# Kernel optimization log

Hardware: AMD Instinct MI355X
Metric: run time of the kernel (lower is better)

## Reference

```python
import jax, jax.numpy as jnp
import numpy as np

DIM = 512
NSLOTS = 8
ITERS = 3
EPS = 1e-8
LN_EPS = 1e-5
SCALE = DIM ** -0.5


def _ln(x, g, b):
    m = jnp.mean(x, axis=-1, keepdims=True)
    v = jnp.mean((x - m) ** 2, axis=-1, keepdims=True)
    return (x - m) / jnp.sqrt(v + LN_EPS) * g + b


def _gru(x, h, W_ih, W_hh, b_ih, b_hh):
    # PyTorch GRUCell, gate order r,z,n
    gi = x @ W_ih.T + b_ih
    gh = h @ W_hh.T + b_hh
    ir, iz, inn = jnp.split(gi, 3, axis=-1)
    hr, hz, hn = jnp.split(gh, 3, axis=-1)
    r = jax.nn.sigmoid(ir + hr)
    z = jax.nn.sigmoid(iz + hz)
    n = jnp.tanh(inn + r * hn)
    return (1.0 - z) * n + z * h


def _norm_attn(dots):
    # softmax over slot axis, then renormalize over token axis
    a = jax.nn.softmax(dots, axis=1)
    return a / (jnp.sum(a, axis=-1, keepdims=True) + EPS)


def setup_inputs() -> dict:
    key = jax.random.key(0)
    ks = jax.random.split(key, 16)
    b, na, ni = 32, 1024, 3136
    d, hd = DIM, DIM  # hidden_dim = max(dim, 128) = 512
    s = 0.02
    inp = {
        'inputs_audio': jax.random.normal(ks[0], (b, na, d), jnp.float32),
        'inputs_image': jax.random.normal(ks[1], (b, ni, d), jnp.float32),
        'slots_noise': jax.random.normal(ks[2], (b, NSLOTS, d), jnp.float32),
        'slots_mu': jax.random.normal(ks[3], (1, 1, d), jnp.float32),
        'slots_logsigma': jnp.zeros((1, 1, d), jnp.float32),
        'ln_in_g': jnp.ones((d,), jnp.float32), 'ln_in_b': jnp.zeros((d,), jnp.float32),
        'ln_slots_g': jnp.ones((d,), jnp.float32), 'ln_slots_b': jnp.zeros((d,), jnp.float32),
        'ln_ff_g': jnp.ones((d,), jnp.float32), 'ln_ff_b': jnp.zeros((d,), jnp.float32),
        'Wq': jax.random.normal(ks[4], (d, d), jnp.float32) * s, 'bq': jnp.zeros((d,), jnp.float32),
        'Wk': jax.random.normal(ks[5], (d, d), jnp.float32) * s, 'bk': jnp.zeros((d,), jnp.float32),
        'Wv': jax.random.normal(ks[6], (d, d), jnp.float32) * s, 'bv': jnp.zeros((d,), jnp.float32),
        'W_ih': jax.random.normal(ks[7], (3 * d, d), jnp.float32) * s,
        'W_hh': jax.random.normal(ks[8], (3 * d, d), jnp.float32) * s,
        'b_ih': jnp.zeros((3 * d,), jnp.float32), 'b_hh': jnp.zeros((3 * d,), jnp.float32),
        'W1': jax.random.normal(ks[9], (hd, d), jnp.float32) * s, 'b1': jnp.zeros((hd,), jnp.float32),
        'W2': jax.random.normal(ks[10], (d, hd), jnp.float32) * s, 'b2': jnp.zeros((d,), jnp.float32),
    }
    return inp


def reference(inputs_audio, inputs_image, slots_noise, slots_mu, slots_logsigma,
              ln_in_g, ln_in_b, ln_slots_g, ln_slots_b, ln_ff_g, ln_ff_b,
              Wq, bq, Wk, bk, Wv, bv, W_ih, W_hh, b_ih, b_hh, W1, b1, W2, b2):
    b, na, d = inputs_audio.shape
    slots0 = slots_mu + jnp.exp(slots_logsigma) * slots_noise  # [b, S, d]

    ia = _ln(inputs_audio, ln_in_g, ln_in_b)
    ii = _ln(inputs_image, ln_in_g, ln_in_b)
    k_a = ia @ Wk.T + bk
    v_a = ia @ Wv.T + bv
    k_i = ii @ Wk.T + bk
    v_i = ii @ Wv.T + bv

    def mlp(x):
        return jax.nn.relu(x @ W1.T + b1) @ W2.T + b2

    def step(slots, k, v):
        prev = slots
        sn = _ln(slots, ln_slots_g, ln_slots_b)
        q = sn @ Wq.T + bq
        dots = jnp.einsum('bid,bjd->bij', q, k) * SCALE
        attn = _norm_attn(dots)
        upd = jnp.einsum('bjd,bij->bid', v, attn)
        h = _gru(upd.reshape(-1, d), prev.reshape(-1, d), W_ih, W_hh, b_ih, b_hh)
        slots = h.reshape(b, -1, d)
        slots = slots + mlp(_ln(slots, ln_ff_g, ln_ff_b))
        return slots, q, attn

    slots_a, slots_i = slots0, slots0
    for _ in range(ITERS):
        slots_a, q_a, attn_a = step(slots_a, k_a, v_a)
        slots_i, q_i, attn_i = step(slots_i, k_i, v_i)

    cross_ai = _norm_attn(jnp.einsum('bid,bjd->bij', q_a, k_i) * SCALE)  # audio->image
    cross_ia = _norm_attn(jnp.einsum('bid,bjd->bij', q_i, k_a) * SCALE)  # image->audio

    return (slots_a, q_a, k_a, attn_a, cross_ia,
            slots_i, q_i, k_i, attn_i, cross_ai)
```

## Files before the change

kernel.cpp:

```cpp
#include <hip/hip_runtime.h>
#include <hip/hip_bf16.h>

#define DIM 512
#define EPS 1e-8f
#define LN_EPS 1e-5f
#define SCALE 0.04419417382415922f

typedef float f32x4 __attribute__((ext_vector_type(4)));
typedef __bf16 bf16;
typedef __bf16 bf16x8 __attribute__((ext_vector_type(8)));

typedef const __attribute__((address_space(1))) void gvoid;
typedef __attribute__((address_space(3))) void lvoid;

__device__ inline float bf2f_lo(unsigned u) { union { unsigned x; float f; } c; c.x = u << 16; return c.f; }
__device__ inline float bf2f_hi(unsigned u) { union { unsigned x; float f; } c; c.x = u & 0xffff0000u; return c.f; }

__global__ __launch_bounds__(256) void k_stats_convert(
    const float* __restrict__ x, bf16* __restrict__ xbf,
    float* __restrict__ stats, int M)
{
  int row = blockIdx.x * 4 + (threadIdx.x >> 6);
  int lane = threadIdx.x & 63;
  if (row >= M) return;
  const float* xr = x + (size_t)row * DIM;
  float4 a = *(const float4*)(xr + lane * 8);
  float4 b = *(const float4*)(xr + lane * 8 + 4);
  float s  = a.x + a.y + a.z + a.w + b.x + b.y + b.z + b.w;
  float ss = a.x*a.x + a.y*a.y + a.z*a.z + a.w*a.w
           + b.x*b.x + b.y*b.y + b.z*b.z + b.w*b.w;
  for (int off = 32; off; off >>= 1) { s += __shfl_xor(s, off); ss += __shfl_xor(ss, off); }
  float mean = s * (1.0f / DIM);
  float var  = ss * (1.0f / DIM) - mean * mean;
  float rs   = rsqrtf(var + LN_EPS);
  if (lane == 0) { stats[row * 2] = mean; stats[row * 2 + 1] = rs; }
  union { bf16 h[8]; uint4 u; } cv;
  cv.h[0] = (bf16)a.x; cv.h[1] = (bf16)a.y; cv.h[2] = (bf16)a.z; cv.h[3] = (bf16)a.w;
  cv.h[4] = (bf16)b.x; cv.h[5] = (bf16)b.y; cv.h[6] = (bf16)b.z; cv.h[7] = (bf16)b.w;
  *(uint4*)(xbf + (size_t)row * DIM + lane * 8) = cv.u;
}

__global__ __launch_bounds__(256) void k_stats512(
    const float* __restrict__ x, float* __restrict__ stats)
{
  int row = blockIdx.x * 4 + (threadIdx.x >> 6);
  int lane = threadIdx.x & 63;
  const float* xr = x + (size_t)row * DIM;
  float4 a = *(const float4*)(xr + lane * 8);
  float4 b = *(const float4*)(xr + lane * 8 + 4);
  float s  = a.x + a.y + a.z + a.w + b.x + b.y + b.z + b.w;
  float ss = a.x*a.x + a.y*a.y + a.z*a.z + a.w*a.w
           + b.x*b.x + b.y*b.y + b.z*b.z + b.w*b.w;
  for (int off = 32; off; off >>= 1) { s += __shfl_xor(s, off); ss += __shfl_xor(ss, off); }
  float mean = s * (1.0f / DIM);
  float rs   = rsqrtf(ss * (1.0f / DIM) - mean * mean + LN_EPS);
  if (lane == 0) { stats[row * 2] = mean; stats[row * 2 + 1] = rs; }
}

__global__ __launch_bounds__(64) void k_prep(
    const float* __restrict__ Wk, const float* __restrict__ bk,
    const float* __restrict__ Wv, const float* __restrict__ bv,
    const float* __restrict__ g_in, const float* __restrict__ b_in,
    const float* __restrict__ Wq, const float* __restrict__ bq,
    const float* __restrict__ g_s, const float* __restrict__ b_s,
    const float* __restrict__ W1, const float* __restrict__ b1,
    const float* __restrict__ g_f, const float* __restrict__ b_f,
    bf16* __restrict__ wbf, float* __restrict__ c1kv, float* __restrict__ c2kv,
    float* __restrict__ Wqp, float* __restrict__ cq1, float* __restrict__ cq2,
    float* __restrict__ W1p, float* __restrict__ cf1, float* __restrict__ cf2)
{
  int n = blockIdx.x; int lane = threadIdx.x;
  if (n < 1024) {
    const float* W = (n < DIM) ? (Wk + (size_t)n * DIM) : (Wv + (size_t)(n - DIM) * DIM);
    float bias = (n < DIM) ? bk[n] : bv[n - DIM];
    float s1 = 0.f, s2 = 0.f;
    union { bf16 h[8]; uint4 u; } cv;
#pragma unroll
    for (int j = 0; j < 8; ++j) {
      int d = lane * 8 + j;
      float w = W[d];
      float gw = g_in[d] * w;
      s1 += gw; s2 += b_in[d] * w;
      cv.h[j] = (bf16)gw;
    }
    *(uint4*)(wbf + (size_t)n * DIM + lane * 8) = cv.u;
    for (int off = 32; off; off >>= 1) { s1 += __shfl_xor(s1, off); s2 += __shfl_xor(s2, off); }
    if (lane == 0) { c1kv[n] = s1; c2kv[n] = s2 + bias; }
  } else {
    int m; const float* W; float bias; const float* g; const float* b;
    float* Wp; float* cc1; float* cc2;
    if (n < 1536) { m = n - 1024; W = Wq + (size_t)m * DIM; bias = bq[m]; g = g_s; b = b_s; Wp = Wqp; cc1 = cq1; cc2 = cq2; }
    else          { m = n - 1536; W = W1 + (size_t)m * DIM; bias = b1[m]; g = g_f; b = b_f; Wp = W1p; cc1 = cf1; cc2 = cf2; }
    float s1 = 0.f, s2 = 0.f;
    float arr[8];
#pragma unroll
    for (int j = 0; j < 8; ++j) {
      int d = lane * 8 + j;
      float w = W[d];
      float gw = g[d] * w;
      s1 += gw; s2 += b[d] * w;
      arr[j] = gw;
    }
    *(float4*)(Wp + (size_t)m * DIM + lane * 8)     = make_float4(arr[0], arr[1], arr[2], arr[3]);
    *(float4*)(Wp + (size_t)m * DIM + lane * 8 + 4) = make_float4(arr[4], arr[5], arr[6], arr[7]);
    for (int off = 32; off; off >>= 1) { s1 += __shfl_xor(s1, off); s2 += __shfl_xor(s2, off); }
    if (lane == 0) { cc1[m] = s1; cc2[m] = s2 + bias; }
  }
}

__global__ __launch_bounds__(256, 4) void k_kv_gemm(
    const bf16* __restrict__ xa, const bf16* __restrict__ xi,
    const bf16* __restrict__ wbf,
    const float* __restrict__ sa, const float* __restrict__ si,
    const float* __restrict__ c1, const float* __restrict__ c2,
    float* __restrict__ ka, float* __restrict__ ki,
    bf16* __restrict__ kba, bf16* __restrict__ kbi,
    bf16* __restrict__ va, bf16* __restrict__ vi,
    int nblkA, int nblkTot)
{
  __shared__ bf16 As[2][128 * 32];
  __shared__ bf16 Bs[2][128 * 32];
  const int t = threadIdx.x, wave = t >> 6, lane = t & 63;
  int bid = blockIdx.x;
  int rid = (bid & 7) * (nblkTot >> 3) + (bid >> 3);
  bool isA = rid < nblkA;
  int lrid = isA ? rid : rid - nblkA;
  const bf16* x = isA ? xa : xi;
  const float* stats = isA ? sa : si;
  float* kout = isA ? ka : ki;
  bf16* kbf = isA ? kba : kbi;
  bf16* vbf = isA ? va : vi;
  const int row0 = (lrid >> 3) * 128, col0 = (lrid & 7) * 128;
  f32x4 acc[4][4] = {};

  const int sr  = wave * 16 + (lane >> 2);
  const int sgl = ((lane & 3) ^ ((lane >> 3) & 3)) * 8;
  const bf16* asrc = x   + (size_t)(row0 + sr) * DIM + sgl;
  const bf16* bsrc = wbf + (size_t)(col0 + sr) * DIM + sgl;

  auto stage = [&](int buf, int k0) {
#pragma unroll
    for (int p = 0; p < 2; ++p) {
      __builtin_amdgcn_global_load_lds(
          (gvoid*)(asrc + (size_t)(p * 64) * DIM + k0),
          (lvoid*)((char*)&As[buf][0] + (p * 256 + wave * 64) * 16), 16, 0, 0);
      __builtin_amdgcn_global_load_lds(
          (gvoid*)(bsrc + (size_t)(p * 64) * DIM + k0),
          (lvoid*)((char*)&Bs[buf][0] + (p * 256 + wave * 64) * 16), 16, 0, 0);
    }
  };

  const int l15 = lane & 15, q16 = lane >> 4;
  const int wm = wave >> 1, wn = wave & 1;
  const int gpx = (q16 ^ ((l15 >> 1) & 3)) * 8;

  stage(0, 0);
  int cur = 0;
  for (int ks = 0; ks < 16; ++ks) {
    __syncthreads();
    if (ks < 15) stage(cur ^ 1, (ks + 1) * 32);
    const bf16* Ab = &As[cur][0];
    const bf16* Bb = &Bs[cur][0];
    bf16x8 ax[4], bw[4];
#pragma unroll
    for (int mi = 0; mi < 4; ++mi)
      ax[mi] = *(const bf16x8*)(Ab + (wm * 64 + mi * 16 + l15) * 32 + gpx);
#pragma unroll
    for (int ni = 0; ni < 4; ++ni)
      bw[ni] = *(const bf16x8*)(Bb + (wn * 64 + ni * 16 + l15) * 32 + gpx);
#pragma unroll
    for (int ni = 0; ni < 4; ++ni)
#pragma unroll
      for (int mi = 0; mi < 4; ++mi)
        acc[ni][mi] = __builtin_amdgcn_mfma_f32_16x16x32_bf16(bw[ni], ax[mi], acc[ni][mi], 0, 0, 0);
    cur ^= 1;
  }

#pragma unroll
  for (int mi = 0; mi < 4; ++mi) {
    int row = row0 + wm * 64 + mi * 16 + l15;
    float2 st = *(const float2*)&stats[row * 2];
    float rs = st.y, rm = st.y * st.x;
#pragma unroll
    for (int ni = 0; ni < 4; ++ni) {
      int col = col0 + wn * 64 + ni * 16 + q16 * 4;
      float4 c1v = *(const float4*)&c1[col];
      float4 c2v = *(const float4*)&c2[col];
      f32x4 a = acc[ni][mi];
      float4 o;
      o.x = rs * a[0] - rm * c1v.x + c2v.x;
      o.y = rs * a[1] - rm * c1v.y + c2v.y;
      o.z = rs * a[2] - rm * c1v.z + c2v.z;
      o.w = rs * a[3] - rm * c1v.w + c2v.w;
      union { bf16 h[4]; uint2 u; } pk;
      pk.h[0] = (bf16)o.x; pk.h[1] = (bf16)o.y; pk.h[2] = (bf16)o.z; pk.h[3] = (bf16)o.w;
      if (col0 < DIM) {
        *(float4*)&kout[(size_t)row * DIM + col] = o;
        if (kbf) *(uint2*)&kbf[(size_t)row * DIM + col] = pk.u;
      } else {
        *(uint2*)&vbf[(size_t)row * DIM + (col - DIM)] = pk.u;
      }
    }
  }
}

__global__ __launch_bounds__(256) void k_f2bf(
    const float* __restrict__ in, bf16* __restrict__ out)
{
  size_t i = ((size_t)blockIdx.x * 256 + threadIdx.x) * 8;
  float4 a = *(const float4*)(in + i);
  float4 b = *(const float4*)(in + i + 4);
  union { bf16 h[8]; uint4 u; } cv;
  cv.h[0] = (bf16)a.x; cv.h[1] = (bf16)a.y; cv.h[2] = (bf16)a.z; cv.h[3] = (bf16)a.w;
  cv.h[4] = (bf16)b.x; cv.h[5] = (bf16)b.y; cv.h[6] = (bf16)b.z; cv.h[7] = (bf16)b.w;
  *(uint4*)(out + i) = cv.u;
}

__global__ __launch_bounds__(256) void k_init_slots(
    const float* __restrict__ noise, const float* __restrict__ mu,
    const float* __restrict__ lsig, float* __restrict__ slots)
{
  int idx = blockIdx.x * 256 + threadIdx.x;
  int d = idx & (DIM - 1);
  float v = mu[d] + expf(lsig[d]) * noise[idx];
  slots[idx] = v;
  slots[131072 + idx] = v;
}

template <int MODE>
__global__ __launch_bounds__(128) void k_sgemm(
    const float* __restrict__ A, const float* __restrict__ B, int N,
    float* __restrict__ C,
    const float* __restrict__ c1a, const float* __restrict__ c2a,
    const float* __restrict__ stats,
    const float* __restrict__ bias, const float* __restrict__ invden,
    const float* __restrict__ R,
    float* __restrict__ outA, float* __restrict__ outI,
    bf16* __restrict__ qbf)
{
  __shared__ float As[32][33];
  __shared__ float Bs[64][33];
  int t = threadIdx.x;
  int m0 = blockIdx.y * 32, n0 = blockIdx.x * 64;
  float acc[4][4] = {};
  for (int k0 = 0; k0 < DIM; k0 += 32) {
    __syncthreads();
#pragma unroll
    for (int p = 0; p < 2; ++p) {
      int idx = p * 128 + t, r = idx >> 3, c4 = (idx & 7) * 4;
      float4 v = *(const float4*)(A + (size_t)(m0 + r) * DIM + k0 + c4);
      As[r][c4] = v.x; As[r][c4 + 1] = v.y; As[r][c4 + 2] = v.z; As[r][c4 + 3] = v.w;
    }
#pragma unroll
    for (int p = 0; p < 4; ++p) {
      int idx = p * 128 + t, r = idx >> 3, c4 = (idx & 7) * 4;
      float4 v = *(const float4*)(B + (size_t)(n0 + r) * DIM + k0 + c4);
      Bs[r][c4] = v.x; Bs[r][c4 + 1] = v.y; Bs[r][c4 + 2] = v.z; Bs[r][c4 + 3] = v.w;
    }
    __syncthreads();
    int tr = t >> 4, tc = t & 15;
#pragma unroll
    for (int k = 0; k < 32; ++k) {
      float a0 = As[tr * 4][k], a1 = As[tr * 4 + 1][k], a2 = As[tr * 4 + 2][k], a3 = As[tr * 4 + 3][k];
      float b0 = Bs[tc * 4][k], b1 = Bs[tc * 4 + 1][k], b2 = Bs[tc * 4 + 2][k], b3 = Bs[tc * 4 + 3][k];
      acc[0][0] += a0 * b0; acc[0][1] += a0 * b1; acc[0][2] += a0 * b2; acc[0][3] += a0 * b3;
      acc[1][0] += a1 * b0; acc[1][1] += a1 * b1; acc[1][2] += a1 * b2; acc[1][3] += a1 * b3;
      acc[2][0] += a2 * b0; acc[2][1] += a2 * b1; acc[2][2] += a2 * b2; acc[2][3] += a2 * b3;
      acc[3][0] += a3 * b0; acc[3][1] += a3 * b1; acc[3][2] += a3 * b2; acc[3][3] += a3 * b3;
    }
  }
  int tr = t >> 4, tc = t & 15;
#pragma unroll
  for (int mi = 0; mi < 4; ++mi) {
    int row = m0 + tr * 4 + mi;
#pragma unroll
    for (int ni = 0; ni < 4; ++ni) {
      int col = n0 + tc * 4 + ni;
      float v = acc[mi][ni];
      if (MODE == 0 || MODE == 3) {
        float mean = stats[row * 2], rs = stats[row * 2 + 1];
        v = rs * v - rs * mean * c1a[col] + c2a[col];
      }
      if (MODE == 1) v = v * invden[row] + bias[col];
      if (MODE == 2 || MODE == 4) v += bias[col];
      if (MODE == 3) v = fmaxf(v, 0.0f);
      if (MODE == 4) v += R[(size_t)row * N + col];
      if (MODE == 0) {
        if (row < 256) outA[(size_t)row * DIM + col] = v;
        else           outI[(size_t)(row - 256) * DIM + col] = v;
        qbf[(size_t)row * DIM + col] = (bf16)(v * SCALE);
      } else {
        C[(size_t)row * N + col] = v;
        if (MODE == 4 && outA) {
          if (row < 256) outA[(size_t)row * DIM + col] = v;
          else           outI[(size_t)(row - 256) * DIM + col] = v;
        }
      }
    }
  }
}

__global__ __launch_bounds__(256) void k_dots(
    const bf16* __restrict__ qA, const bf16* __restrict__ qI,
    const bf16* __restrict__ kA, const bf16* __restrict__ kI,
    float* __restrict__ aoutA, float* __restrict__ aoutI,
    float* __restrict__ denp, int NA_, int NI_)
{
  __shared__ bf16 ks[128 * 64];
  __shared__ float dsh[32];
  int t = threadIdx.x, wave = t >> 6, lane = t & 63;
  int b = blockIdx.y, tile = blockIdx.x;
  bool isA = tile < 8;
  int til = isA ? tile : tile - 8;
  int N = isA ? NA_ : NI_;
  int j0 = til * 128;
  const bf16* q = (isA ? qA : qI) + (size_t)b * 8 * DIM;
  const bf16* k = (isA ? kA : kI) + (size_t)b * N * DIM;
  float* aout = (isA ? aoutA : aoutI) + (size_t)b * 8 * N;
  int drow = (isA ? 0 : 256) + b * 8;

  const int l15 = lane & 15, q16 = lane >> 4;
  bf16x8 afq[16];
  {
    const bf16* qr = q + (size_t)(l15 & 7) * DIM + q16 * 8;
#pragma unroll
    for (int f = 0; f < 16; ++f)
      afq[f] = *(const bf16x8*)(qr + f * 32);
  }

  const int sr  = wave * 8 + (lane >> 3);
  const int sgl = ((lane & 7) ^ (lane >> 3)) * 8;
  f32x4 acc[2] = {};
  for (int c = 0; c < 8; ++c) {
    __syncthreads();
#pragma unroll
    for (int p = 0; p < 4; ++p) {
      int jr = j0 + p * 32 + sr;
      if (jr > N - 1) jr = N - 1;
      __builtin_amdgcn_global_load_lds(
          (gvoid*)(k + (size_t)jr * DIM + c * 64 + sgl),
          (lvoid*)((char*)ks + (p * 256 + wave * 64) * 16), 16, 0, 0);
    }
    __syncthreads();
#pragma unroll
    for (int kk = 0; kk < 2; ++kk) {
#pragma unroll
      for (int n = 0; n < 2; ++n) {
        int R = wave * 32 + n * 16 + l15;
        int gp = (kk * 4 + q16) ^ (R & 7);
        bf16x8 bfr = *(const bf16x8*)(ks + R * 64 + gp * 8);
        acc[n] = __builtin_amdgcn_mfma_f32_16x16x32_bf16(afq[c * 2 + kk], bfr, acc[n], 0, 0, 0);
      }
    }
  }

  float dsum[8];
#pragma unroll
  for (int i = 0; i < 8; ++i) dsum[i] = 0.f;
#pragma unroll
  for (int n = 0; n < 2; ++n) {
    int j = j0 + wave * 32 + n * 16 + l15;
    float dv[8];
#pragma unroll
    for (int r = 0; r < 4; ++r) {
      float own = acc[n][r];
      float oth = __shfl_xor(own, 16);
      if (q16 == 0) { dv[r] = own; dv[4 + r] = oth; }
      else          { dv[r] = oth; dv[4 + r] = own; }
    }
    float mx = dv[0];
#pragma unroll
    for (int i = 1; i < 8; ++i) mx = fmaxf(mx, dv[i]);
    float sum = 0.f;
#pragma unroll
    for (int i = 0; i < 8; ++i) { dv[i] = __expf(dv[i] - mx); sum += dv[i]; }
    float inv = 1.0f / sum;
    bool valid = (j < N);
#pragma unroll
    for (int i = 0; i < 8; ++i) {
      float av = valid ? dv[i] * inv : 0.0f;
      dsum[i] += av;
      if (valid && q16 == 0) aout[(size_t)i * N + j] = av;
    }
  }
#pragma unroll
  for (int i = 0; i < 8; ++i) {
    float v = dsum[i];
    v += __shfl_xor(v, 1); v += __shfl_xor(v, 2);
    v += __shfl_xor(v, 4); v += __shfl_xor(v, 8);
    dsum[i] = v;
  }
  if (lane == 0) {
#pragma unroll
    for (int i = 0; i < 8; ++i) dsh[wave * 8 + i] = dsum[i];
  }
  __syncthreads();
  if (t < 8) {
    float den = dsh[t] + dsh[8 + t] + dsh[16 + t] + dsh[24 + t];
    denp[((size_t)drow + t) * 32 + til] = den;
  }
}

__global__ __launch_bounds__(256) void k_upd(
    const bf16* __restrict__ vA, const bf16* __restrict__ vI,
    const float* __restrict__ aA, const float* __restrict__ aI,
    float* __restrict__ numpA, float* __restrict__ numpI, int NA_, int NI_)
{
  __shared__ float ash[128 * 12];
  int t = threadIdx.x, b = blockIdx.y, x = blockIdx.x;
  bool isA = x < 4;
  int c = isA ? x : x - 4;
  int N = isA ? NA_ : NI_;
  int nc = isA ? 4 : 13;
  int jstart = c * 256;
  int jend = jstart + 256; if (jend > N) jend = N;
  const bf16* v = (isA ? vA : vI) + (size_t)b * N * DIM;
  const float* a = (isA ? aA : aI) + (size_t)b * 8 * N;
  float acc[16] = {};
  int d0 = t * 2;
  for (int jt = jstart; jt < jend; jt += 128) {
    int jmax = jend - jt; if (jmax > 128) jmax = 128;
    __syncthreads();
    {
      int i = t >> 5, jq = (t & 31) * 4;
      float4 av = make_float4(0.f, 0.f, 0.f, 0.f);
      if (jt + jq < N) av = *(const float4*)&a[(size_t)i * N + jt + jq];
      ash[(jq + 0) * 12 + i] = av.x;
      ash[(jq + 1) * 12 + i] = av.y;
      ash[(jq + 2) * 12 + i] = av.z;
      ash[(jq + 3) * 12 + i] = av.w;
    }
    __syncthreads();
    for (int jj = 0; jj < jmax; ++jj) {
      unsigned vv = *(const unsigned*)(v + (size_t)(jt + jj) * DIM + d0);
      float v0 = bf2f_lo(vv), v1 = bf2f_hi(vv);
      float4 a0 = *(const float4*)&ash[jj * 12];
      float4 a1 = *(const float4*)&ash[jj * 12 + 4];
      acc[0]  += a0.x * v0; acc[1]  += a0.x * v1;
      acc[2]  += a0.y * v0; acc[3]  += a0.y * v1;
      acc[4]  += a0.z * v0; acc[5]  += a0.z * v1;
      acc[6]  += a0.w * v0; acc[7]  += a0.w * v1;
      acc[8]  += a1.x * v0; acc[9]  += a1.x * v1;
      acc[10] += a1.y * v0; acc[11] += a1.y * v1;
      acc[12] += a1.z * v0; acc[13] += a1.z * v1;
      acc[14] += a1.w * v0; acc[15] += a1.w * v1;
    }
  }
  float* np = (isA ? numpA : numpI) + (((size_t)b * nc + c) * 8) * DIM;
#pragma unroll
  for (int i = 0; i < 8; ++i)
    *(float2*)&np[(size_t)i * DIM + d0] = make_float2(acc[i * 2], acc[i * 2 + 1]);
}

__global__ __launch_bounds__(256) void k_numred(
    const float* __restrict__ numpA, const float* __restrict__ numpI,
    const float* __restrict__ denp,
    float* __restrict__ num, float* __restrict__ invden)
{
  int m = blockIdx.x, t = threadIdx.x;
  bool isA = m < 256;
  int mm = isA ? m : m - 256;
  int bb = mm >> 3, i = mm & 7;
  int nc = isA ? 4 : 13;
  const float* np = (isA ? numpA : numpI) + (((size_t)bb * nc) * 8 + i) * DIM;
  int d0 = t * 2;
  float s0 = 0.f, s1 = 0.f;
  for (int c = 0; c < nc; ++c) {
    float2 vv = *(const float2*)&np[(size_t)c * 8 * DIM + d0];
    s0 += vv.x; s1 += vv.y;
  }
  *(float2*)&num[(size_t)m * DIM + d0] = make_float2(s0, s1);
  if (t == 0) {
    int nch = isA ? 8 : 25;
    float den = EPS;
    for (int c2 = 0; c2 < nch; ++c2) den += denp[(size_t)m * 32 + c2];
    invden[m] = 1.0f / den;
  }
}

__global__ __launch_bounds__(256) void k_gru(
    const float* __restrict__ gi, const float* __restrict__ gh,
    const float* __restrict__ prev,
    float* __restrict__ hout, float* __restrict__ stats_h)
{
  int m = blockIdx.x; int t = threadIdx.x;
  size_t b3 = (size_t)m * 1536, b1 = (size_t)m * DIM;
  float h[2]; float s = 0.f, ss = 0.f;
#pragma unroll
  for (int p = 0; p < 2; ++p) {
    int d = t + p * 256;
    float ir = gi[b3 + d], iz = gi[b3 + 512 + d], in_ = gi[b3 + 1024 + d];
    float hr = gh[b3 + d], hz = gh[b3 + 512 + d], hn = gh[b3 + 1024 + d];
    float r = 1.f / (1.f + __expf(-(ir + hr)));
    float z = 1.f / (1.f + __expf(-(iz + hz)));
    float n = tanhf(in_ + r * hn);
    float hv = (1.f - z) * n + z * prev[b1 + d];
    hout[b1 + d] = hv;
    h[p] = hv; s += hv; ss += hv * hv;
  }
  for (int off = 32; off; off >>= 1) { s += __shfl_xor(s, off); ss += __shfl_xor(ss, off); }
  __shared__ float red[8];
  int wv = t >> 6, ln = t & 63;
  if (ln == 0) { red[wv] = s; red[4 + wv] = ss; }
  __syncthreads();
  s = red[0] + red[1] + red[2] + red[3];
  ss = red[4] + red[5] + red[6] + red[7];
  float mean = s * (1.0f / DIM);
  float rs = rsqrtf(ss * (1.0f / DIM) - mean * mean + LN_EPS);
  if (t == 0) { stats_h[m * 2] = mean; stats_h[m * 2 + 1] = rs; }
}

__global__ __launch_bounds__(256) void k_renorm2(
    const float* __restrict__ aA, const float* __restrict__ aI,
    const float* __restrict__ denp,
    float* __restrict__ outA, float* __restrict__ outI, int NA_, int NI_)
{
  int m = blockIdx.x; int t = threadIdx.x;
  bool isA = m < 256;
  int mm = isA ? m : m - 256;
  int N = isA ? NA_ : NI_;
  int nch = isA ? 8 : 25;
  const float* in = (isA ? aA : aI) + (size_t)mm * N;
  float* out = (isA ? outA : outI) + (size_t)mm * N;
  float den = EPS;
  for (int c = 0; c < nch; ++c) den += denp[(size_t)m * 32 + c];
  float inv = 1.0f / den;
  for (int idx = t; idx * 4 < N; idx += 256) {
    float4 v = *(const float4*)&in[idx * 4];
    v.x *= inv; v.y *= inv; v.z *= inv; v.w *= inv;
    *(float4*)&out[idx * 4] = v;
  }
}

extern "C" void kernel_launch(void* const* d_in, const int* in_sizes, int n_in,
                              void* d_out, int out_size, void* d_ws, size_t ws_size,
                              hipStream_t stream)
{
  (void)in_sizes; (void)n_in; (void)out_size;
  const float* x_a   = (const float*)d_in[0];
  const float* x_i   = (const float*)d_in[1];
  const float* noise = (const float*)d_in[2];
  const float* mu    = (const float*)d_in[3];
  const float* lsig  = (const float*)d_in[4];
  const float* ln_in_g = (const float*)d_in[5];
  const float* ln_in_b = (const float*)d_in[6];
  const float* ln_s_g  = (const float*)d_in[7];
  const float* ln_s_b  = (const float*)d_in[8];
  const float* ln_f_g  = (const float*)d_in[9];
  const float* ln_f_b  = (const float*)d_in[10];
  const float* Wq = (const float*)d_in[11]; const float* bq = (const float*)d_in[12];
  const float* Wk = (const float*)d_in[13]; const float* bk = (const float*)d_in[14];
  const float* Wv = (const float*)d_in[15]; const float* bv = (const float*)d_in[16];
  const float* W_ih = (const float*)d_in[17]; const float* W_hh = (const float*)d_in[18];
  const float* b_ih = (const float*)d_in[19]; const float* b_hh = (const float*)d_in[20];
  const float* W1 = (const float*)d_in[21]; const float* b1 = (const float*)d_in[22];
  const float* W2 = (const float*)d_in[23]; const float* b2 = (const float*)d_in[24];

  const int NA = 1024, NI = 3136;
  const int MA = 32 * NA, MI = 32 * NI;

  float* out = (float*)d_out;
  float* o_slots_a  = out;
  float* o_q_a      = out + 131072;
  float* o_k_a      = out + 262144;
  float* o_attn_a   = out + 17039360;
  float* o_cross_ia = out + 17301504;
  float* o_slots_i  = out + 17563648;
  float* o_q_i      = out + 17694720;
  float* o_k_i      = out + 17825792;
  float* o_attn_i   = out + 69206016;
  float* o_cross_ai = out + 70008832;

  char* w = (char*)d_ws;
  size_t used = 0;
  auto alloc = [&](size_t bytes) {
    char* p = w + used;
    used += (bytes + 255) & ~(size_t)255;
    return p;
  };
  bf16* xbf_a = (bf16*)alloc((size_t)MA * DIM * 2);
  bf16* xbf_i = (bf16*)alloc((size_t)MI * DIM * 2);
  bf16* vbf_a = (bf16*)alloc((size_t)MA * DIM * 2);
  bf16* vbf_i = (bf16*)alloc((size_t)MI * DIM * 2);
  float* stats_a = (float*)alloc((size_t)MA * 2 * 4);
  float* stats_i = (float*)alloc((size_t)MI * 2 * 4);
  bf16* wbf  = (bf16*)alloc(1024 * 512 * 2);
  float* c1kv = (float*)alloc(1024 * 4);
  float* c2kv = (float*)alloc(1024 * 4);
  float* Wqp = (float*)alloc(512 * 512 * 4);
  float* cq1 = (float*)alloc(512 * 4);
  float* cq2 = (float*)alloc(512 * 4);
  float* W1p = (float*)alloc(512 * 512 * 4);
  float* cf1 = (float*)alloc(512 * 4);
  float* cf2 = (float*)alloc(512 * 4);
  float* slots = (float*)alloc(512 * 512 * 4);
  bf16*  qbf   = (bf16*)alloc(512 * 512 * 2);
  float* mid   = (float*)alloc(512 * 512 * 4);
  float* hid   = (float*)alloc(512 * 512 * 4);
  float* num   = (float*)alloc(512 * 512 * 4);
  float* gib   = (float*)alloc(512 * 1536 * 4);
  float* ghb   = (float*)alloc(512 * 1536 * 4);
  float* stats_s = (float*)alloc(512 * 2 * 4);
  float* stats_h = (float*)alloc(512 * 2 * 4);
  float* invden  = (float*)alloc(512 * 4);
  float* denp    = (float*)alloc(512 * 32 * 4);
  float* abuf_a  = (float*)alloc((size_t)256 * NA * 4);
  float* abuf_i  = (float*)alloc((size_t)256 * NI * 4);
  float* numpA   = (float*)alloc((size_t)32 * 4 * 8 * DIM * 4);
  float* numpI   = (float*)alloc((size_t)32 * 13 * 8 * DIM * 4);
  if (used > ws_size) return;

  size_t kbf_bytes = (((size_t)MA * DIM * 2 + 255) & ~(size_t)255)
                   + (((size_t)MI * DIM * 2 + 255) & ~(size_t)255);
  bf16* kbf_a; bf16* kbf_i; bool kbf_fused;
  if (used + kbf_bytes <= ws_size) {
    kbf_a = (bf16*)alloc((size_t)MA * DIM * 2);
    kbf_i = (bf16*)alloc((size_t)MI * DIM * 2);
    kbf_fused = true;
  } else {
    kbf_a = xbf_a; kbf_i = xbf_i;
    kbf_fused = false;
  }

  k_stats_convert<<<MA / 4, 256, 0, stream>>>(x_a, xbf_a, stats_a, MA);
  k_stats_convert<<<MI / 4, 256, 0, stream>>>(x_i, xbf_i, stats_i, MI);
  k_prep<<<2048, 64, 0, stream>>>(Wk, bk, Wv, bv, ln_in_g, ln_in_b,
                                  Wq, bq, ln_s_g, ln_s_b, W1, b1, ln_f_g, ln_f_b,
                                  wbf, c1kv, c2kv, Wqp, cq1, cq2, W1p, cf1, cf2);
  {
    int nblkA = (MA / 128) * 8;
    int nblkTot = nblkA + (MI / 128) * 8;
    k_kv_gemm<<<nblkTot, 256, 0, stream>>>(xbf_a, xbf_i, wbf, stats_a, stats_i,
        c1kv, c2kv, o_k_a, o_k_i,
        kbf_fused ? kbf_a : nullptr, kbf_fused ? kbf_i : nullptr,
        vbf_a, vbf_i, nblkA, nblkTot);
  }
  if (!kbf_fused) {
    k_f2bf<<<MA * DIM / 2048, 256, 0, stream>>>(o_k_a, kbf_a);
    k_f2bf<<<MI * DIM / 2048, 256, 0, stream>>>(o_k_i, kbf_i);
  }
  k_init_slots<<<512, 256, 0, stream>>>(noise, mu, lsig, slots);
  k_stats512<<<128, 256, 0, stream>>>(slots, stats_s);

  for (int it = 0; it < 3; ++it) {
    bool last = (it == 2);
    k_sgemm<0><<<dim3(8, 16), 128, 0, stream>>>(slots, Wqp, DIM, nullptr,
        cq1, cq2, stats_s, nullptr, nullptr, nullptr, o_q_a, o_q_i, qbf);
    k_dots<<<dim3(33, 32), 256, 0, stream>>>(qbf, qbf + 256 * DIM,
        kbf_a, kbf_i, abuf_a, abuf_i, denp, NA, NI);
    k_upd<<<dim3(17, 32), 256, 0, stream>>>(vbf_a, vbf_i, abuf_a, abuf_i, numpA, numpI, NA, NI);
    k_numred<<<512, 256, 0, stream>>>(numpA, numpI, denp, num, invden);
    k_sgemm<1><<<dim3(24, 16), 128, 0, stream>>>(num, W_ih, 1536, gib,
        nullptr, nullptr, nullptr, b_ih, invden, nullptr, nullptr, nullptr, nullptr);
    k_sgemm<2><<<dim3(24, 16), 128, 0, stream>>>(slots, W_hh, 1536, ghb,
        nullptr, nullptr, nullptr, b_hh, nullptr, nullptr, nullptr, nullptr, nullptr);
    k_gru<<<512, 256, 0, stream>>>(gib, ghb, slots, mid, stats_h);
    k_sgemm<3><<<dim3(8, 16), 128, 0, stream>>>(mid, W1p, DIM, hid,
        cf1, cf2, stats_h, nullptr, nullptr, nullptr, nullptr, nullptr, nullptr);
    k_sgemm<4><<<dim3(8, 16), 128, 0, stream>>>(hid, W2, DIM, slots,
        nullptr, nullptr, nullptr, b2, nullptr, mid,
        last ? o_slots_a : nullptr, last ? o_slots_i : nullptr, nullptr);
    if (!last) k_stats512<<<128, 256, 0, stream>>>(slots, stats_s);
  }

  k_renorm2<<<512, 256, 0, stream>>>(abuf_a, abuf_i, denp, o_attn_a, o_attn_i, NA, NI);

  k_dots<<<dim3(33, 32), 256, 0, stream>>>(qbf + 256 * DIM, qbf,
      kbf_a, kbf_i, abuf_a, abuf_i, denp, NA, NI);
  k_renorm2<<<512, 256, 0, stream>>>(abuf_a, abuf_i, denp, o_cross_ia, o_cross_ai, NA, NI);
}
```

Before: 1.217 ms.

## Deepen prefetch in projection GEMM and dots, merge GRU gate GEMMs into one launch

The bf16 MFMA projection GEMM and the k_dots kernel now prefetch two stages ahead. Each waits with explicit vmcnt waits and scheduling barriers instead of a sync-load-sync loop, so global-to-LDS loads overlap MFMA work. k_dots gets a double-buffered LDS tile and precomputes its clamped source pointers. The two GRU gate SGEMMs (input and hidden) are merged into one k_gates launch with twice the blocks, which removes a launch and fills more CUs. The cost is extra LDS use and fragile hand-written waitcnt logic.

```diff
diff --git a/kernel.cpp b/kernel.cpp
--- a/kernel.cpp
+++ b/kernel.cpp
@@ -15,6 +15,10 @@
 
 __device__ inline float bf2f_lo(unsigned u) { union { unsigned x; float f; } c; c.x = u << 16; return c.f; }
 __device__ inline float bf2f_hi(unsigned u) { union { unsigned x; float f; } c; c.x = u & 0xffff0000u; return c.f; }
+
+#define SBAR() do { __builtin_amdgcn_sched_barrier(0); \
+                    __builtin_amdgcn_s_barrier(); \
+                    __builtin_amdgcn_sched_barrier(0); } while (0)
 
 __global__ __launch_bounds__(256) void k_stats_convert(
     const float* __restrict__ x, bf16* __restrict__ xbf,
@@ -155,10 +159,11 @@
   const int gpx = (q16 ^ ((l15 >> 1) & 3)) * 8;
 
   stage(0, 0);
+  stage(1, 32);
+  asm volatile("s_waitcnt vmcnt(4)" ::: "memory");
+  SBAR();
   int cur = 0;
   for (int ks = 0; ks < 16; ++ks) {
-    __syncthreads();
-    if (ks < 15) stage(cur ^ 1, (ks + 1) * 32);
     const bf16* Ab = &As[cur][0];
     const bf16* Bb = &Bs[cur][0];
     bf16x8 ax[4], bw[4];
@@ -173,6 +178,15 @@
 #pragma unroll
       for (int mi = 0; mi < 4; ++mi)
         acc[ni][mi] = __builtin_amdgcn_mfma_f32_16x16x32_bf16(bw[ni], ax[mi], acc[ni][mi], 0, 0, 0);
+    SBAR();
+    if (ks < 14) {
+      stage(cur, (ks + 2) * 32);
+      asm volatile("s_waitcnt vmcnt(4)" ::: "memory");
+      SBAR();
+    } else if (ks == 14) {
+      asm volatile("s_waitcnt vmcnt(0)" ::: "memory");
+      SBAR();
+    }
     cur ^= 1;
   }
 
@@ -281,8 +295,7 @@
         float mean = stats[row * 2], rs = stats[row * 2 + 1];
         v = rs * v - rs * mean * c1a[col] + c2a[col];
       }
-      if (MODE == 1) v = v * invden[row] + bias[col];
-      if (MODE == 2 || MODE == 4) v += bias[col];
+      if (MODE == 4) v += bias[col];
       if (MODE == 3) v = fmaxf(v, 0.0f);
       if (MODE == 4) v += R[(size_t)row * N + col];
       if (MODE == 0) {
@@ -300,13 +313,70 @@
   }
 }
 
+__global__ __launch_bounds__(128) void k_gates(
+    const float* __restrict__ num, const float* __restrict__ slots,
+    const float* __restrict__ Wih, const float* __restrict__ Whh,
+    const float* __restrict__ bih, const float* __restrict__ bhh,
+    const float* __restrict__ invden,
+    float* __restrict__ gib, float* __restrict__ ghb)
+{
+  bool first = blockIdx.x < 24;
+  const float* A = first ? num : slots;
+  const float* B = first ? Wih : Whh;
+  const float* bias = first ? bih : bhh;
+  float* C = first ? gib : ghb;
+  int n0 = (first ? blockIdx.x : blockIdx.x - 24) * 64;
+  int m0 = blockIdx.y * 32;
+  __shared__ float As[32][33];
+  __shared__ float Bs[64][33];
+  int t = threadIdx.x;
+  float acc[4][4] = {};
+  for (int k0 = 0; k0 < DIM; k0 += 32) {
+    __syncthreads();
+#pragma unroll
+    for (int p = 0; p < 2; ++p) {
+      int idx = p * 128 + t, r = idx >> 3, c4 = (idx & 7) * 4;
+      float4 v = *(const float4*)(A + (size_t)(m0 + r) * DIM + k0 + c4);
+      As[r][c4] = v.x; As[r][c4 + 1] = v.y; As[r][c4 + 2] = v.z; As[r][c4 + 3] = v.w;
+    }
+#pragma unroll
+    for (int p = 0; p < 4; ++p) {
+      int idx = p * 128 + t, r = idx >> 3, c4 = (idx & 7) * 4;
+      float4 v = *(const float4*)(B + (size_t)(n0 + r) * DIM + k0 + c4);
+      Bs[r][c4] = v.x; Bs[r][c4 + 1] = v.y; Bs[r][c4 + 2] = v.z; Bs[r][c4 + 3] = v.w;
+    }
+    __syncthreads();
+    int tr = t >> 4, tc = t & 15;
+#pragma unroll
+    for (int k = 0; k < 32; ++k) {
+      float a0 = As[tr * 4][k], a1 = As[tr * 4 + 1][k], a2 = As[tr * 4 + 2][k], a3 = As[tr * 4 + 3][k];
+      float b0 = Bs[tc * 4][k], b1 = Bs[tc * 4 + 1][k], b2 = Bs[tc * 4 + 2][k], b3 = Bs[tc * 4 + 3][k];
+      acc[0][0] += a0 * b0; acc[0][1] += a0 * b1; acc[0][2] += a0 * b2; acc[0][3] += a0 * b3;
+      acc[1][0] += a1 * b0; acc[1][1] += a1 * b1; acc[1][2] += a1 * b2; acc[1][3] += a1 * b3;
+      acc[2][0] += a2 * b0; acc[2][1] += a2 * b1; acc[2][2] += a2 * b2; acc[2][3] += a2 * b3;
+      acc[3][0] += a3 * b0; acc[3][1] += a3 * b1; acc[3][2] += a3 * b2; acc[3][3] += a3 * b3;
+    }
+  }
+  int tr = t >> 4, tc = t & 15;
+#pragma unroll
+  for (int mi = 0; mi < 4; ++mi) {
+    int row = m0 + tr * 4 + mi;
+    float sc = first ? invden[row] : 1.0f;
+#pragma unroll
+    for (int ni = 0; ni < 4; ++ni) {
+      int col = n0 + tc * 4 + ni;
+      C[(size_t)row * 1536 + col] = acc[mi][ni] * sc + bias[col];
+    }
+  }
+}
+
 __global__ __launch_bounds__(256) void k_dots(
     const bf16* __restrict__ qA, const bf16* __restrict__ qI,
     const bf16* __restrict__ kA, const bf16* __restrict__ kI,
     float* __restrict__ aoutA, float* __restrict__ aoutI,
     float* __restrict__ denp, int NA_, int NI_)
 {
-  __shared__ bf16 ks[128 * 64];
+  __shared__ bf16 ks[2][128 * 64];
   __shared__ float dsh[32];
   int t = threadIdx.x, wave = t >> 6, lane = t & 63;
   int b = blockIdx.y, tile = blockIdx.x;
@@ -330,28 +400,53 @@
 
   const int sr  = wave * 8 + (lane >> 3);
   const int sgl = ((lane & 7) ^ (lane >> 3)) * 8;
+  int jr = j0 + sr; if (jr > N - 1) jr = N - 1;
+  const bf16* ksrc = k + (size_t)jr * DIM + sgl;
+  int jr2 = j0 + 32 + sr; if (jr2 > N - 1) jr2 = N - 1;
+  const bf16* ksrc2 = k + (size_t)jr2 * DIM + sgl;
+  int jr3 = j0 + 64 + sr; if (jr3 > N - 1) jr3 = N - 1;
+  const bf16* ksrc3 = k + (size_t)jr3 * DIM + sgl;
+  int jr4 = j0 + 96 + sr; if (jr4 > N - 1) jr4 = N - 1;
+  const bf16* ksrc4 = k + (size_t)jr4 * DIM + sgl;
+
+  auto stage = [&](int buf, int c) {
+    __builtin_amdgcn_global_load_lds((gvoid*)(ksrc  + c * 64),
+        (lvoid*)((char*)&ks[buf][0] + (0 * 256 + wave * 64) * 16), 16, 0, 0);
+    __builtin_amdgcn_global_load_lds((gvoid*)(ksrc2 + c * 64),
+        (lvoid*)((char*)&ks[buf][0] + (1 * 256 + wave * 64) * 16), 16, 0, 0);
+    __builtin_amdgcn_global_load_lds((gvoid*)(ksrc3 + c * 64),
+        (lvoid*)((char*)&ks[buf][0] + (2 * 256 + wave * 64) * 16), 16, 0, 0);
+    __builtin_amdgcn_global_load_lds((gvoid*)(ksrc4 + c * 64),
+        (lvoid*)((char*)&ks[buf][0] + (3 * 256 + wave * 64) * 16), 16, 0, 0);
+  };
+
+  stage(0, 0);
+  stage(1, 1);
+  asm volatile("s_waitcnt vmcnt(4)" ::: "memory");
+  SBAR();
   f32x4 acc[2] = {};
+  int cur = 0;
   for (int c = 0; c < 8; ++c) {
-    __syncthreads();
-#pragma unroll
-    for (int p = 0; p < 4; ++p) {
-      int jr = j0 + p * 32 + sr;
-      if (jr > N - 1) jr = N - 1;
-      __builtin_amdgcn_global_load_lds(
-          (gvoid*)(k + (size_t)jr * DIM + c * 64 + sgl),
-          (lvoid*)((char*)ks + (p * 256 + wave * 64) * 16), 16, 0, 0);
-    }
-    __syncthreads();
 #pragma unroll
     for (int kk = 0; kk < 2; ++kk) {
 #pragma unroll
       for (int n = 0; n < 2; ++n) {
         int R = wave * 32 + n * 16 + l15;
         int gp = (kk * 4 + q16) ^ (R & 7);
-        bf16x8 bfr = *(const bf16x8*)(ks + R * 64 + gp * 8);
+        bf16x8 bfr = *(const bf16x8*)(&ks[cur][0] + R * 64 + gp * 8);
         acc[n] = __builtin_amdgcn_mfma_f32_16x16x32_bf16(afq[c * 2 + kk], bfr, acc[n], 0, 0, 0);
       }
     }
+    SBAR();
+    if (c < 6) {
+      stage(cur, c + 2);
+      asm volatile("s_waitcnt vmcnt(4)" ::: "memory");
+      SBAR();
+    } else if (c == 6) {
+      asm volatile("s_waitcnt vmcnt(0)" ::: "memory");
+      SBAR();
+    }
+    cur ^= 1;
   }
 
   float dsum[8];
@@ -650,10 +745,8 @@
         kbf_a, kbf_i, abuf_a, abuf_i, denp, NA, NI);
     k_upd<<<dim3(17, 32), 256, 0, stream>>>(vbf_a, vbf_i, abuf_a, abuf_i, numpA, numpI, NA, NI);
     k_numred<<<512, 256, 0, stream>>>(numpA, numpI, denp, num, invden);
-    k_sgemm<1><<<dim3(24, 16), 128, 0, stream>>>(num, W_ih, 1536, gib,
-        nullptr, nullptr, nullptr, b_ih, invden, nullptr, nullptr, nullptr, nullptr);
-    k_sgemm<2><<<dim3(24, 16), 128, 0, stream>>>(slots, W_hh, 1536, ghb,
-        nullptr, nullptr, nullptr, b_hh, nullptr, nullptr, nullptr, nullptr, nullptr);
+    k_gates<<<dim3(48, 16), 128, 0, stream>>>(num, slots, W_ih, W_hh,
+        b_ih, b_hh, invden, gib, ghb);
     k_gru<<<512, 256, 0, stream>>>(gib, ghb, slots, mid, stats_h);
     k_sgemm<3><<<dim3(8, 16), 128, 0, stream>>>(mid, W1p, DIM, hid,
         cf1, cf2, stats_h, nullptr, nullptr, nullptr, nullptr, nullptr, nullptr);
```

After: 1.111 ms. 8.7% less time.
